# Kernel tuning notes

Measured on AMD Instinct MI355X. Metric: run time of the kernel, lower is better.

The kernel has to match this reference:

```python
import jax, jax.numpy as jnp
import numpy as np

# Model constants (match init_kwargs and fla GatedLinearAttention defaults used in source)
L = 4            # num_layers
D = 1024         # d_model
H = 4            # n_heads
DK = 128         # head key dim  = 0.5*D / H
DV = 256         # head value dim = 1.0*D / H
KD = H * DK      # total key dim = 512
VD = H * DV      # total value dim = 1024
V = 32000        # vocab
B, T = 1, 2048
LR = 16          # gate_low_rank_dim
GLN = 16.0       # gate_logit_normalizer
EPS = 1e-5
SCALE = DK ** -0.5


def setup_inputs() -> dict:
    key = jax.random.key(0)
    ks = jax.random.split(key, 12)
    s = 0.02
    return {
        "input_ids": jax.random.randint(ks[0], (B, T), 0, V),
        "emb": jax.random.normal(ks[1], (V, D), jnp.float32) * s,
        "Wq": jax.random.normal(ks[2], (L, D, KD), jnp.float32) * s,
        "Wk": jax.random.normal(ks[3], (L, D, KD), jnp.float32) * s,
        "Wv": jax.random.normal(ks[4], (L, D, VD), jnp.float32) * s,
        "Wg": jax.random.normal(ks[5], (L, D, VD), jnp.float32) * s,
        "Wgk1": jax.random.normal(ks[6], (L, D, LR), jnp.float32) * s,
        "Wgk2": jax.random.normal(ks[7], (L, LR, KD), jnp.float32) * s,
        "bgk": jnp.zeros((L, KD), jnp.float32),
        "gnw": jnp.ones((L, DV), jnp.float32),
        "Wo": jax.random.normal(ks[8], (L, VD, D), jnp.float32) * s,
        "ln_w": jnp.ones((D,), jnp.float32),
        "ln_b": jnp.zeros((D,), jnp.float32),
        "Wlm": jax.random.normal(ks[9], (D, V), jnp.float32) * s,
        "blm": jnp.zeros((V,), jnp.float32),
    }


def _gla_layer(x, wq, wk, wv, wg, wg1, wg2, bg, nw, wo):
    # x: [B, T, D]
    b, t, _ = x.shape
    q = (x @ wq).reshape(b, t, H, DK) * SCALE
    k = (x @ wk).reshape(b, t, H, DK)
    v = (x @ wv).reshape(b, t, H, DV)
    g = (x @ wg).reshape(b, t, H, DV)
    # low-rank forget gate, log-space, normalized
    gk = (jax.nn.log_sigmoid((x @ wg1) @ wg2 + bg) / GLN).reshape(b, t, H, DK)

    # time-major for scan: [T, B, H, *]
    qt, kt, vt, gkt = (jnp.moveaxis(a, 1, 0) for a in (q, k, v, gk))

    def step(S, inp):
        q_t, k_t, v_t, gk_t = inp  # [B,H,DK], [B,H,DK], [B,H,DV], [B,H,DK]
        S = S * jnp.exp(gk_t)[..., None] + k_t[..., None] * v_t[..., None, :]
        o_t = jnp.einsum('bhk,bhkv->bhv', q_t, S)
        return S, o_t

    S0 = jnp.zeros((b, H, DK, DV), x.dtype)
    _, o = jax.lax.scan(step, S0, (qt, kt, vt, gkt))
    o = jnp.moveaxis(o, 0, 1)  # [B, T, H, DV]
    # fused RMSNorm + swish output gate
    o = o * jax.lax.rsqrt(jnp.mean(o * o, axis=-1, keepdims=True) + EPS) * nw
    o = o * (g * jax.nn.sigmoid(g))
    return o.reshape(b, t, VD) @ wo


def reference(input_ids, emb, Wq, Wk, Wv, Wg, Wgk1, Wgk2, bgk, gnw, Wo, ln_w, ln_b, Wlm, blm):
    h = emb[input_ids]  # [B, T, D]
    for i in range(L):
        h = _gla_layer(h, Wq[i], Wk[i], Wv[i], Wg[i], Wgk1[i], Wgk2[i], bgk[i], gnw[i], Wo[i])
    mu = jnp.mean(h, axis=-1, keepdims=True)
    var = jnp.mean((h - mu) ** 2, axis=-1, keepdims=True)
    h = (h - mu) * jax.lax.rsqrt(var + EPS) * ln_w + ln_b
    return h @ Wlm + blm
```

## Files before the change

### kernel.cpp

```cpp
#include <hip/hip_runtime.h>
#include <hip/hip_bf16.h>
#include <math.h>

#define NL 4
#define TT 2048
#define DD 1024
#define KDIM 512
#define VDIM 1024
#define QSTR 3072
#define NH 4
#define DKH 128
#define DVH 256
#define CH 64
#define NCH 32
#define VOCAB 32000
#define SCALE_Q 0.08838834764831845f

typedef short bf16x8 __attribute__((ext_vector_type(8)));
typedef float f32x4 __attribute__((ext_vector_type(4)));

__device__ __forceinline__ void gload_lds16(const void* g, void* l) {
    __builtin_amdgcn_global_load_lds((const __attribute__((address_space(1))) void*)g,
                                     (__attribute__((address_space(3))) void*)l, 16, 0, 0);
}

__device__ __forceinline__ void store_bf16x4(__hip_bfloat16* p, float a, float b, float c, float d) {
    union { __hip_bfloat16 h[4]; ushort4 v; } r;
    r.h[0] = __float2bfloat16(a); r.h[1] = __float2bfloat16(b);
    r.h[2] = __float2bfloat16(c); r.h[3] = __float2bfloat16(d);
    *(ushort4*)p = r.v;
}

__global__ __launch_bounds__(256) void embed_kernel(const int* __restrict__ ids,
                                                    const float* __restrict__ emb,
                                                    float* __restrict__ h,
                                                    __hip_bfloat16* __restrict__ hb) {
    int idx = blockIdx.x * 256 + threadIdx.x;
    int t = idx >> 8, c4 = idx & 255;
    float4 v = *(const float4*)(emb + (size_t)ids[t] * DD + c4 * 4);
    *(float4*)(h + (size_t)t * DD + c4 * 4) = v;
    store_bf16x4(hb + (size_t)t * DD + c4 * 4, v.x, v.y, v.z, v.w);
}

__global__ __launch_bounds__(256) void tconv_kernel(const float* __restrict__ in,
                                                    __hip_bfloat16* __restrict__ out,
                                                    int K, int N) {
    __shared__ float tle[64][65];
    const int n0 = blockIdx.x * 64, k0 = blockIdx.y * 64;
    const int tid = threadIdx.x;
    const int ty = tid >> 4, tx = tid & 15;
#pragma unroll
    for (int u = 0; u < 4; u++) {
        int r = ty + u * 16;
        float4 v = *(const float4*)(in + (size_t)(k0 + r) * N + n0 + tx * 4);
        tle[r][tx * 4 + 0] = v.x; tle[r][tx * 4 + 1] = v.y;
        tle[r][tx * 4 + 2] = v.z; tle[r][tx * 4 + 3] = v.w;
    }
    __syncthreads();
#pragma unroll
    for (int u = 0; u < 4; u++) {
        int nn = u * 16 + ty;
        store_bf16x4(out + (size_t)(n0 + nn) * K + k0 + tx * 4,
                     tle[tx * 4 + 0][nn], tle[tx * 4 + 1][nn],
                     tle[tx * 4 + 2][nn], tle[tx * 4 + 3][nn]);
    }
}

__global__ __launch_bounds__(256) void tconv_layer_kernel(const float* __restrict__ wq,
                                                          const float* __restrict__ wk,
                                                          const float* __restrict__ wv,
                                                          const float* __restrict__ wg,
                                                          const float* __restrict__ wo,
                                                          __hip_bfloat16* __restrict__ Wt,
                                                          __hip_bfloat16* __restrict__ WoT) {
    __shared__ float tle[64][65];
    int b = blockIdx.x;
    const float* src; __hip_bfloat16* dst; int N, local;
    if (b < 128)      { src = wq; dst = Wt;                         N = 512;  local = b; }
    else if (b < 256) { src = wk; dst = Wt + (size_t)512 * 1024;    N = 512;  local = b - 128; }
    else if (b < 512) { src = wv; dst = Wt + (size_t)1024 * 1024;   N = 1024; local = b - 256; }
    else if (b < 768) { src = wg; dst = Wt + (size_t)2048 * 1024;   N = 1024; local = b - 512; }
    else              { src = wo; dst = WoT;                        N = 1024; local = b - 768; }
    int nbx = N >> 6;
    int n0 = (local % nbx) * 64, k0 = (local / nbx) * 64;
    const int tid = threadIdx.x;
    const int ty = tid >> 4, tx = tid & 15;
#pragma unroll
    for (int u = 0; u < 4; u++) {
        int r = ty + u * 16;
        float4 v = *(const float4*)(src + (size_t)(k0 + r) * N + n0 + tx * 4);
        tle[r][tx * 4 + 0] = v.x; tle[r][tx * 4 + 1] = v.y;
        tle[r][tx * 4 + 2] = v.z; tle[r][tx * 4 + 3] = v.w;
    }
    __syncthreads();
#pragma unroll
    for (int u = 0; u < 4; u++) {
        int nn = u * 16 + ty;
        store_bf16x4(dst + (size_t)(n0 + nn) * 1024 + k0 + tx * 4,
                     tle[tx * 4 + 0][nn], tle[tx * 4 + 1][nn],
                     tle[tx * 4 + 2][nn], tle[tx * 4 + 3][nn]);
    }
}

template<int NF>
__global__ __launch_bounds__(256) void gemm_bf16_db(const __hip_bfloat16* __restrict__ A,
                                                    const __hip_bfloat16* __restrict__ Bt,
                                                    const float* __restrict__ bias,
                                                    float* __restrict__ C,
                                                    __hip_bfloat16* __restrict__ Cb,
                                                    int M, int N, int K) {
    __shared__ short a_lds[2][128 * 32];
    __shared__ short b_lds[2][NF * 32 * 32];
    const int tid = threadIdx.x;
    const int wv = tid >> 6, lane = tid & 63;
    const int wr = wv >> 1, wc = wv & 1;
    const int nbx = gridDim.x;
    int wg = blockIdx.y * nbx + blockIdx.x;
    int cpx = (nbx * gridDim.y) >> 3;
    int swz = (wg & 7) * cpx + (wg >> 3);
    const int m0 = (swz % nbx) * 128, n0 = (swz / nbx) * (NF * 32);
    const int lr = lane & 15, lk = (lane >> 4) * 8;

    f32x4 acc[4][NF];
#pragma unroll
    for (int m = 0; m < 4; m++)
#pragma unroll
        for (int n = 0; n < NF; n++) acc[m][n] = (f32x4)(0.f);

    auto STAGE = [&](int buf, int k0) {
#pragma unroll
        for (int u = 0; u < 2; u++) {
            int s = wv * 128 + u * 64 + lane;
            int r = s >> 2, kc = (s & 3) * 8;
            gload_lds16(A + (size_t)(m0 + r) * K + k0 + kc,
                        &a_lds[buf][(wv * 128 + u * 64) * 8]);
        }
        if constexpr (NF == 4) {
#pragma unroll
            for (int u = 0; u < 2; u++) {
                int s = wv * 128 + u * 64 + lane;
                int r = s >> 2, kc = (s & 3) * 8;
                gload_lds16(Bt + (size_t)(n0 + r) * K + k0 + kc,
                            &b_lds[buf][(wv * 128 + u * 64) * 8]);
            }
        } else {
            int s = wv * 64 + lane;
            int r = s >> 2, kc = (s & 3) * 8;
            gload_lds16(Bt + (size_t)(n0 + r) * K + k0 + kc,
                        &b_lds[buf][(wv * 64) * 8]);
        }
    };
    auto COMPUTE = [&](int buf) {
        bf16x8 af[4], bfr[NF];
#pragma unroll
        for (int m = 0; m < 4; m++)
            af[m] = *(const bf16x8*)&a_lds[buf][(wr * 64 + m * 16 + lr) * 32 + lk];
#pragma unroll
        for (int n = 0; n < NF; n++)
            bfr[n] = *(const bf16x8*)&b_lds[buf][(wc * (NF * 16) + n * 16 + lr) * 32 + lk];
#pragma unroll
        for (int m = 0; m < 4; m++)
#pragma unroll
            for (int n = 0; n < NF; n++)
                acc[m][n] = __builtin_amdgcn_mfma_f32_16x16x32_bf16(af[m], bfr[n], acc[m][n], 0, 0, 0);
    };

    STAGE(0, 0);
    __syncthreads();
    int cur = 0;
    for (int k0 = 32; k0 < K; k0 += 32) {
        STAGE(cur ^ 1, k0);
        COMPUTE(cur);
        __syncthreads();
        cur ^= 1;
    }
    COMPUTE(cur);

    const int rbase = (lane >> 4) * 4;
#pragma unroll
    for (int n = 0; n < NF; n++) {
        int col = n0 + wc * (NF * 16) + n * 16 + lr;
        float bv = bias ? bias[col] : 0.f;
#pragma unroll
        for (int m = 0; m < 4; m++) {
            int row = m0 + wr * 64 + m * 16 + rbase;
#pragma unroll
            for (int r = 0; r < 4; r++) {
                float val = acc[m][n][r] + bv;
                C[(size_t)(row + r) * N + col] = val;
                if (Cb) Cb[(size_t)(row + r) * N + col] = __float2bfloat16(val);
            }
        }
    }
}

__device__ __forceinline__ void lm_stage(const __hip_bfloat16* src, int row0,
                                         char* dst, int kt32, int wv, int lane, int K) {
#pragma unroll
    for (int ii = 0; ii < 2; ii++) {
        int o = (wv * 2 + ii) * 1024;
        int ob = o + lane * 16;
        int lg = ob ^ (((ob >> 7) & 7) << 4);
        int row = lg >> 6;
        int ce = (lg & 63) >> 1;
        gload_lds16(src + (size_t)(row0 + row) * K + kt32 * 32 + ce, dst + o);
    }
}

__device__ __forceinline__ bf16x8 lm_frag(const char* sub, int row, int lk2) {
    int lg = ((row >> 1) << 7) + ((row & 1) << 6) + lk2;
    return *(const bf16x8*)(sub + (lg ^ (((row >> 1) & 7) << 4)));
}

template<int PT, bool LOADB, int VM>
__device__ __forceinline__ void lm_phase(const char* aT, const char* bT,
                                         const __hip_bfloat16* ssrc, int srow0,
                                         char* sdst, int skt32,
                                         bf16x8 (&bfr)[4][2], f32x4 (&acc)[8][4],
                                         int wr, int wc, int lr, int lk2,
                                         int wv, int lane, int K) {
    if constexpr (LOADB) {
#pragma unroll
        for (int n = 0; n < 4; n++)
#pragma unroll
            for (int ks = 0; ks < 2; ks++)
                bfr[n][ks] = lm_frag(bT + ks * 16384, wc * 64 + n * 16 + lr, lk2);
    }
    bf16x8 af[2][2];
#pragma unroll
    for (int mm = 0; mm < 2; mm++)
#pragma unroll
        for (int ks = 0; ks < 2; ks++)
            af[mm][ks] = lm_frag(aT + ks * 16384, wr * 128 + (2 * PT + mm) * 16 + lr, lk2);
    lm_stage(ssrc, srow0, sdst, skt32, wv, lane, K);
    asm volatile("s_barrier" ::: "memory");
    __builtin_amdgcn_s_setprio(1);
#pragma unroll
    for (int mm = 0; mm < 2; mm++)
#pragma unroll
        for (int n = 0; n < 4; n++) {
            acc[2 * PT + mm][n] = __builtin_amdgcn_mfma_f32_16x16x32_bf16(af[mm][0], bfr[n][0], acc[2 * PT + mm][n], 0, 0, 0);
            acc[2 * PT + mm][n] = __builtin_amdgcn_mfma_f32_16x16x32_bf16(af[mm][1], bfr[n][1], acc[2 * PT + mm][n], 0, 0, 0);
        }
    __builtin_amdgcn_s_setprio(0);
    if constexpr (VM == 4) asm volatile("s_waitcnt vmcnt(4)" ::: "memory");
    asm volatile("s_barrier" ::: "memory");
}

__global__ __launch_bounds__(512, 1) void gemm256_lm(const __hip_bfloat16* __restrict__ A,
                                                     const __hip_bfloat16* __restrict__ Bt,
                                                     const float* __restrict__ bias,
                                                     float* __restrict__ C,
                                                     int M, int N, int K) {
    extern __shared__ __align__(16) char smem[];
    char* sA0 = smem;
    char* sA1 = smem + 32768;
    char* sB0 = smem + 65536;
    char* sB1 = smem + 98304;
    const int tid = threadIdx.x;
    const int wv = tid >> 6, lane = tid & 63;
    const int wr = wv >> 2, wc = wv & 3;
    const int lr = lane & 15, lk2 = (lane >> 4) * 16;

    const int nbx = gridDim.x;
    int wg = blockIdx.y * nbx + blockIdx.x;
    int cpx = (nbx * gridDim.y) >> 3;
    int swz = (wg & 7) * cpx + (wg >> 3);
    const int m0 = (swz % nbx) * 256;
    const int n0 = (swz / nbx) * 256;

    f32x4 acc[8][4];
#pragma unroll
    for (int m = 0; m < 8; m++)
#pragma unroll
        for (int n = 0; n < 4; n++) acc[m][n] = (f32x4)(0.f);

    const int NTI = K / 64;
    const int NI  = NTI / 2;

    lm_stage(A,  m0, sA0 + 0,     0, wv, lane, K);
    lm_stage(A,  m0, sA0 + 16384, 1, wv, lane, K);
    lm_stage(Bt, n0, sB0 + 0,     0, wv, lane, K);
    lm_stage(Bt, n0, sB0 + 16384, 1, wv, lane, K);
    lm_stage(Bt, n0, sB1 + 0,     2, wv, lane, K);
    lm_stage(Bt, n0, sB1 + 16384, 3, wv, lane, K);
    asm volatile("s_waitcnt vmcnt(0)" ::: "memory");
    asm volatile("s_barrier" ::: "memory");

    for (int i = 0; i < NI; i++) {
        int tOdd = 2 * i + 1;
        int tE   = 2 * i + 2 < NTI ? 2 * i + 2 : NTI - 1;
        int tB3  = 2 * i + 3 < NTI ? 2 * i + 3 : NTI - 1;
        bf16x8 bfr[4][2];
        lm_phase<0, true , 0>(sA0, sB0, A,  m0, sA1 + 0,     2 * tOdd + 0, bfr, acc, wr, wc, lr, lk2, wv, lane, K);
        lm_phase<1, false, 0>(sA0, sB0, A,  m0, sA1 + 16384, 2 * tOdd + 1, bfr, acc, wr, wc, lr, lk2, wv, lane, K);
        lm_phase<2, false, 0>(sA0, sB0, Bt, n0, sB0 + 0,     2 * tE   + 0, bfr, acc, wr, wc, lr, lk2, wv, lane, K);
        lm_phase<3, false, 4>(sA0, sB0, Bt, n0, sB0 + 16384, 2 * tE   + 1, bfr, acc, wr, wc, lr, lk2, wv, lane, K);
        lm_phase<0, true , 0>(sA1, sB1, A,  m0, sA0 + 0,     2 * tE   + 0, bfr, acc, wr, wc, lr, lk2, wv, lane, K);
        lm_phase<1, false, 0>(sA1, sB1, A,  m0, sA0 + 16384, 2 * tE   + 1, bfr, acc, wr, wc, lr, lk2, wv, lane, K);
        lm_phase<2, false, 0>(sA1, sB1, Bt, n0, sB1 + 0,     2 * tB3  + 0, bfr, acc, wr, wc, lr, lk2, wv, lane, K);
        lm_phase<3, false, 4>(sA1, sB1, Bt, n0, sB1 + 16384, 2 * tB3  + 1, bfr, acc, wr, wc, lr, lk2, wv, lane, K);
    }

    const int r4 = (lane >> 4) * 4;
#pragma unroll
    for (int n = 0; n < 4; n++) {
        int col = n0 + wc * 64 + n * 16 + lr;
        float bv = bias ? bias[col] : 0.f;
#pragma unroll
        for (int m = 0; m < 8; m++) {
            int row = m0 + wr * 128 + m * 16 + r4;
#pragma unroll
            for (int r = 0; r < 4; r++)
                C[(size_t)(row + r) * N + col] = acc[m][n][r] + bv;
        }
    }
}

__global__ __launch_bounds__(256) void lowrank1_kernel(const float* __restrict__ h,
                                                       const float* __restrict__ W1,
                                                       float* __restrict__ xg) {
    int t = blockIdx.x;
    int tid = threadIdx.x;
    int j = tid & 15, ks = tid >> 4;
    const float* hr = h + (size_t)t * DD + ks * 64;
    const float* w = W1 + (size_t)(ks * 64) * 16 + j;
    float acc = 0.f;
#pragma unroll 8
    for (int kk = 0; kk < 64; kk++) acc = fmaf(hr[kk], w[kk * 16], acc);
    __shared__ float red[16][17];
    red[ks][j] = acc;
    __syncthreads();
    if (tid < 16) {
        float s = 0.f;
#pragma unroll
        for (int r = 0; r < 16; r++) s += red[r][tid];
        xg[t * 16 + tid] = s;
    }
}

__global__ __launch_bounds__(256) void lowrank2_kernel(const float* __restrict__ xg,
                                                       const float* __restrict__ W2,
                                                       const float* __restrict__ bg,
                                                       float* __restrict__ gk) {
    int idx = blockIdx.x * 256 + threadIdx.x;
    int t = idx >> 9, n = idx & 511;
    const float* xr = xg + t * 16;
    float s = bg[n];
#pragma unroll
    for (int r = 0; r < 16; r++) s = fmaf(xr[r], W2[r * KDIM + n], s);
    float ls = fminf(s, 0.f) - log1pf(expf(-fabsf(s)));
    gk[idx] = ls * (1.f / 16.f);
}

__global__ __launch_bounds__(256) void gatescan_kernel(const float* __restrict__ qkvg,
                                                       const float* __restrict__ gk,
                                                       float* __restrict__ Gl,
                                                       __hip_bfloat16* __restrict__ qhB,
                                                       __hip_bfloat16* __restrict__ khB,
                                                       __hip_bfloat16* __restrict__ ktT) {
    int idx = blockIdx.x * 256 + threadIdx.x;
    int c = idx >> 9, col = idx & 511;
    float G = 0.f;
    float kh[64];
#pragma unroll
    for (int t = 0; t < 64; t++) {
        G += gk[(size_t)(c * 64 + t) * KDIM + col];
        const float* qp = qkvg + (size_t)(c * 64 + t) * QSTR + col;
        float qv = qp[0], kv = qp[512];
        qhB[(size_t)(c * 64 + t) * KDIM + col] = __float2bfloat16(qv * expf(G) * SCALE_Q);
        float khv = kv * expf(-G);
        khB[(size_t)(c * 64 + t) * KDIM + col] = __float2bfloat16(khv);
        kh[t] = khv;
    }
    Gl[idx] = G;
    float eGl = expf(G);
    int hh = col >> 7, dk = col & 127;
    __hip_bfloat16* kp = ktT + ((size_t)(c * NH + hh) * DKH + dk) * CH;
#pragma unroll
    for (int t = 0; t < 64; t++) kp[t] = __float2bfloat16(kh[t] * eGl);
}

__global__ __launch_bounds__(256) void vtrans_kernel(const float* __restrict__ qkvg,
                                                     __hip_bfloat16* __restrict__ vT) {
    __shared__ float tle[64][65];
    int bid = blockIdx.x;
    int dvq = bid & 3, hh = (bid >> 2) & 3, c = bid >> 4;
    int tid = threadIdx.x, ty = tid >> 4, tx = tid & 15;
#pragma unroll
    for (int u = 0; u < 4; u++) {
        int r = u * 16 + ty;
        float4 v = *(const float4*)(qkvg + (size_t)(c * 64 + r) * QSTR + 1024 + hh * DVH + dvq * 64 + tx * 4);
        tle[r][tx * 4 + 0] = v.x; tle[r][tx * 4 + 1] = v.y;
        tle[r][tx * 4 + 2] = v.z; tle[r][tx * 4 + 3] = v.w;
    }
    __syncthreads();
    __hip_bfloat16* dst = vT + ((size_t)(c * NH + hh) * DVH + dvq * 64) * CH;
#pragma unroll
    for (int u = 0; u < 4; u++) {
        int dv = u * 16 + ty;
        store_bf16x4(dst + (size_t)dv * CH + tx * 4,
                     tle[tx * 4 + 0][dv], tle[tx * 4 + 1][dv],
                     tle[tx * 4 + 2][dv], tle[tx * 4 + 3][dv]);
    }
}

__global__ __launch_bounds__(256) void chunkU_mfma(const __hip_bfloat16* __restrict__ vT,
                                                   const __hip_bfloat16* __restrict__ ktT,
                                                   __hip_bfloat16* __restrict__ U) {
    const int ch = blockIdx.x;
    const __hip_bfloat16* Ap = vT + (size_t)ch * DVH * CH;
    const __hip_bfloat16* Bp = ktT + (size_t)ch * DKH * CH;
    __hip_bfloat16* Cp = U + (size_t)ch * DVH * DKH;
    const int tid = threadIdx.x, wv = tid >> 6, lane = tid & 63;
    const int wr = wv >> 1, wc = wv & 1;
    const int lr = lane & 15, lk = (lane >> 4) * 8;
    f32x4 acc[8][4];
#pragma unroll
    for (int m = 0; m < 8; m++)
#pragma unroll
        for (int n = 0; n < 4; n++) acc[m][n] = (f32x4)(0.f);
#pragma unroll
    for (int ks = 0; ks < 2; ks++) {
        bf16x8 a[8], b[4];
#pragma unroll
        for (int m = 0; m < 8; m++)
            a[m] = *(const bf16x8*)(Ap + (size_t)(wr * 128 + m * 16 + lr) * CH + ks * 32 + lk);
#pragma unroll
        for (int n = 0; n < 4; n++)
            b[n] = *(const bf16x8*)(Bp + (size_t)(wc * 64 + n * 16 + lr) * CH + ks * 32 + lk);
#pragma unroll
        for (int m = 0; m < 8; m++)
#pragma unroll
            for (int n = 0; n < 4; n++)
                acc[m][n] = __builtin_amdgcn_mfma_f32_16x16x32_bf16(a[m], b[n], acc[m][n], 0, 0, 0);
    }
    const int r4 = (lane >> 4) * 4;
#pragma unroll
    for (int m = 0; m < 8; m++)
#pragma unroll
        for (int n = 0; n < 4; n++)
#pragma unroll
            for (int r = 0; r < 4; r++)
                Cp[(size_t)(wr * 128 + m * 16 + r4 + r) * DKH + wc * 64 + n * 16 + lr] =
                    __float2bfloat16(acc[m][n][r]);
}

__global__ __launch_bounds__(256) void scan_states_kernel(__hip_bfloat16* __restrict__ U,
                                                          const float* __restrict__ Gl) {
    int idx = blockIdx.x * 256 + threadIdx.x;
    int hh = idx >> 15, dv = (idx >> 7) & 255, dk = idx & 127;
    int col = hh * DKH + dk;
    float s = 0.f;
    for (int c = 0; c < NCH; c++) {
        __hip_bfloat16* p = U + ((size_t)(c * NH + hh) * DVH + dv) * DKH + dk;
        float u = __bfloat162float(*p);
        *p = __float2bfloat16(s);
        s = s * expf(Gl[c * KDIM + col]) + u;
    }
}

__global__ __launch_bounds__(256) void attn_rms_mfma(const __hip_bfloat16* __restrict__ qhB,
                                                     const __hip_bfloat16* __restrict__ khB,
                                                     const __hip_bfloat16* __restrict__ vT,
                                                     const __hip_bfloat16* __restrict__ Ub,
                                                     const float* __restrict__ qkvg,
                                                     const float* __restrict__ nw,
                                                     __hip_bfloat16* __restrict__ obb) {
    __shared__ __hip_bfloat16 P[32 * 72];
    __shared__ float sums[32][2];
    const int bid = blockIdx.x;
    const int rh = bid & 1, hh = (bid >> 1) & 3, c = bid >> 3;
    const int t0 = c * CH;
    const int tid = threadIdx.x, wv = tid >> 6, lane = tid & 63;
    const int half = wv >> 1, rg = wv & 1;
    const int lr = lane & 15, lk = (lane >> 4) * 8;
    const int r4 = (lane >> 4) * 4;
    const int rr = rh * 32 + rg * 16;

    bf16x8 qf[4];
#pragma unroll
    for (int ks = 0; ks < 4; ks++)
        qf[ks] = *(const bf16x8*)(qhB + (size_t)(t0 + rr + lr) * KDIM + hh * DKH + ks * 32 + lk);

    if (half == 0) {
        f32x4 s[4];
#pragma unroll
        for (int n = 0; n < 4; n++) s[n] = (f32x4)(0.f);
#pragma unroll
        for (int n = 0; n < 4; n++)
#pragma unroll
            for (int ks = 0; ks < 4; ks++) {
                bf16x8 kf = *(const bf16x8*)(khB + (size_t)(t0 + n * 16 + lr) * KDIM + hh * DKH + ks * 32 + lk);
                s[n] = __builtin_amdgcn_mfma_f32_16x16x32_bf16(qf[ks], kf, s[n], 0, 0, 0);
            }
#pragma unroll
        for (int n = 0; n < 4; n++)
#pragma unroll
            for (int r = 0; r < 4; r++) {
                int i = rr + r4 + r, j = n * 16 + lr;
                float val = (j <= i) ? s[n][r] : 0.f;
                P[(rg * 16 + r4 + r) * 72 + j] = __float2bfloat16(val);
            }
    }
    __syncthreads();

    const __hip_bfloat16* vTp = vT + ((size_t)(c * NH + hh) * DVH + half * 128) * CH;
    const __hip_bfloat16* Ubp = Ub + ((size_t)(c * NH + hh) * DVH + half * 128) * DKH;
    bf16x8 pf[2];
#pragma unroll
    for (int ks = 0; ks < 2; ks++)
        pf[ks] = *(const bf16x8*)&P[(rg * 16 + lr) * 72 + ks * 32 + lk];

    f32x4 o[8];
#pragma unroll
    for (int n = 0; n < 8; n++) o[n] = (f32x4)(0.f);
#pragma unroll
    for (int n = 0; n < 8; n++) {
#pragma unroll
        for (int ks = 0; ks < 2; ks++) {
            bf16x8 vf = *(const bf16x8*)(vTp + (size_t)(n * 16 + lr) * CH + ks * 32 + lk);
            o[n] = __builtin_amdgcn_mfma_f32_16x16x32_bf16(pf[ks], vf, o[n], 0, 0, 0);
        }
#pragma unroll
        for (int ks = 0; ks < 4; ks++) {
            bf16x8 uf = *(const bf16x8*)(Ubp + (size_t)(n * 16 + lr) * DKH + ks * 32 + lk);
            o[n] = __builtin_amdgcn_mfma_f32_16x16x32_bf16(qf[ks], uf, o[n], 0, 0, 0);
        }
    }

    float part[4];
#pragma unroll
    for (int r = 0; r < 4; r++) {
        float p = 0.f;
#pragma unroll
        for (int n = 0; n < 8; n++) p = fmaf(o[n][r], o[n][r], p);
        part[r] = p;
    }
#pragma unroll
    for (int off = 1; off < 16; off <<= 1)
#pragma unroll
        for (int r = 0; r < 4; r++) part[r] += __shfl_xor(part[r], off);
    if (lr == 0)
#pragma unroll
        for (int r = 0; r < 4; r++) sums[rg * 16 + r4 + r][half] = part[r];
    __syncthreads();

#pragma unroll
    for (int r = 0; r < 4; r++) {
        int lrow = rg * 16 + r4 + r;
        int t = t0 + rh * 32 + lrow;
        float tot = sums[lrow][0] + sums[lrow][1];
        float rinv = rsqrtf(tot * (1.f / 256.f) + 1e-5f);
#pragma unroll
        for (int n = 0; n < 8; n++) {
            int col = half * 128 + n * 16 + lr;
            float gv = qkvg[(size_t)t * QSTR + 2048 + hh * DVH + col];
            float val = o[n][r] * rinv * nw[col] * (gv / (1.f + expf(-gv)));
            obb[(size_t)t * VDIM + hh * DVH + col] = __float2bfloat16(val);
        }
    }
}

__global__ __launch_bounds__(256) void ln_kernel(const float* __restrict__ h,
                                                 const float* __restrict__ w,
                                                 const float* __restrict__ b,
                                                 __hip_bfloat16* __restrict__ out16) {
    int t = blockIdx.x;
    int tid = threadIdx.x;
    float4 x = *(const float4*)(h + (size_t)t * DD + tid * 4);
    float s = x.x + x.y + x.z + x.w;
    float ss = x.x * x.x + x.y * x.y + x.z * x.z + x.w * x.w;
#pragma unroll
    for (int off = 32; off > 0; off >>= 1) {
        s += __shfl_xor(s, off);
        ss += __shfl_xor(ss, off);
    }
    __shared__ float rs[4], rss[4];
    int wv = tid >> 6;
    if ((tid & 63) == 0) { rs[wv] = s; rss[wv] = ss; }
    __syncthreads();
    s = rs[0] + rs[1] + rs[2] + rs[3];
    ss = rss[0] + rss[1] + rss[2] + rss[3];
    float mu = s * (1.f / 1024.f);
    float var = ss * (1.f / 1024.f) - mu * mu;
    float r = rsqrtf(var + 1e-5f);
    float4 wv4 = *(const float4*)(w + tid * 4);
    float4 bv4 = *(const float4*)(b + tid * 4);
    store_bf16x4(out16 + (size_t)t * DD + tid * 4,
                 (x.x - mu) * r * wv4.x + bv4.x,
                 (x.y - mu) * r * wv4.y + bv4.y,
                 (x.z - mu) * r * wv4.z + bv4.z,
                 (x.w - mu) * r * wv4.w + bv4.w);
}

extern "C" void kernel_launch(void* const* d_in, const int* in_sizes, int n_in,
                              void* d_out, int out_size, void* d_ws, size_t ws_size,
                              hipStream_t stream) {
    const int*   ids  = (const int*)d_in[0];
    const float* emb  = (const float*)d_in[1];
    const float* Wq   = (const float*)d_in[2];
    const float* Wk   = (const float*)d_in[3];
    const float* Wv   = (const float*)d_in[4];
    const float* Wg   = (const float*)d_in[5];
    const float* Wgk1 = (const float*)d_in[6];
    const float* Wgk2 = (const float*)d_in[7];
    const float* bgk  = (const float*)d_in[8];
    const float* gnw  = (const float*)d_in[9];
    const float* Wo   = (const float*)d_in[10];
    const float* lnw  = (const float*)d_in[11];
    const float* lnb  = (const float*)d_in[12];
    const float* Wlm  = (const float*)d_in[13];
    const float* blm  = (const float*)d_in[14];
    float* out = (float*)d_out;

    float* ws = (float*)d_ws;
    float* h    = ws; ws += (size_t)TT * DD;
    float* qkvg = ws; ws += (size_t)TT * QSTR;
    float* gk   = ws; ws += (size_t)TT * KDIM;
    float* xg   = ws; ws += (size_t)TT * 16;
    float* Gl   = ws; ws += (size_t)NCH * KDIM;
    __hip_bfloat16* hb    = (__hip_bfloat16*)ws; ws += (size_t)TT * DD / 2;
    __hip_bfloat16* obb   = (__hip_bfloat16*)ws; ws += (size_t)TT * DD / 2;
    __hip_bfloat16* lnb16 = (__hip_bfloat16*)ws; ws += (size_t)TT * DD / 2;
    __hip_bfloat16* qhB   = (__hip_bfloat16*)ws; ws += (size_t)TT * KDIM / 2;
    __hip_bfloat16* khB   = (__hip_bfloat16*)ws; ws += (size_t)TT * KDIM / 2;
    __hip_bfloat16* ktT   = (__hip_bfloat16*)ws; ws += (size_t)NCH * NH * DKH * CH / 2;
    __hip_bfloat16* vT    = (__hip_bfloat16*)ws; ws += (size_t)NCH * NH * DVH * CH / 2;
    __hip_bfloat16* Ub    = (__hip_bfloat16*)ws; ws += (size_t)NCH * NH * DVH * DKH / 2;
    __hip_bfloat16* Wt    = (__hip_bfloat16*)ws; ws += (size_t)QSTR * DD / 2;
    __hip_bfloat16* WoT   = (__hip_bfloat16*)ws; ws += (size_t)VDIM * DD / 2;
    __hip_bfloat16* WlmT  = (__hip_bfloat16*)ws; ws += (size_t)VOCAB * DD / 2;

    hipFuncSetAttribute((const void*)gemm256_lm,
                        hipFuncAttributeMaxDynamicSharedMemorySize, 131072);

    embed_kernel<<<TT, 256, 0, stream>>>(ids, emb, h, hb);
    tconv_kernel<<<dim3(VOCAB / 64, DD / 64), 256, 0, stream>>>(Wlm, WlmT, DD, VOCAB);

    for (int l = 0; l < NL; l++) {
        const float* w1 = Wgk1 + (size_t)l * DD * 16;
        const float* w2 = Wgk2 + (size_t)l * 16 * KDIM;
        const float* bg = bgk + (size_t)l * KDIM;
        const float* nw = gnw + (size_t)l * DVH;

        tconv_layer_kernel<<<1024, 256, 0, stream>>>(Wq + (size_t)l * DD * KDIM,
                                                     Wk + (size_t)l * DD * KDIM,
                                                     Wv + (size_t)l * DD * VDIM,
                                                     Wg + (size_t)l * DD * VDIM,
                                                     Wo + (size_t)l * VDIM * DD, Wt, WoT);
        gemm_bf16_db<4><<<dim3(TT / 128, QSTR / 128), 256, 0, stream>>>(hb, Wt, nullptr, qkvg, nullptr, TT, QSTR, DD);
        lowrank1_kernel<<<TT, 256, 0, stream>>>(h, w1, xg);
        lowrank2_kernel<<<TT * KDIM / 256, 256, 0, stream>>>(xg, w2, bg, gk);
        gatescan_kernel<<<NCH * KDIM / 256, 256, 0, stream>>>(qkvg, gk, Gl, qhB, khB, ktT);
        vtrans_kernel<<<NCH * NH * 4, 256, 0, stream>>>(qkvg, vT);
        chunkU_mfma<<<NCH * NH, 256, 0, stream>>>(vT, ktT, Ub);
        scan_states_kernel<<<NH * DVH * DKH / 256, 256, 0, stream>>>(Ub, Gl);
        attn_rms_mfma<<<NCH * NH * 2, 256, 0, stream>>>(qhB, khB, vT, Ub, qkvg, nw, obb);
        gemm_bf16_db<2><<<dim3(TT / 128, DD / 64), 256, 0, stream>>>(obb, WoT, nullptr, h, hb, TT, DD, VDIM);
    }

    ln_kernel<<<TT, 256, 0, stream>>>(h, lnw, lnb, lnb16);
    gemm256_lm<<<dim3(TT / 256, VOCAB / 256), 512, 131072, stream>>>(lnb16, WlmT, blm, out, TT, VOCAB, DD);
}
```

Measured before the change: 706.1 us.

## Fuse low-rank gate projection into chunked gate scan and relax LM-head vmcnt wait

Merges the second low-rank gate kernel into the gate cumulative-sum kernel. Each block now computes log-sigmoid gates for a 64-token chunk and 64 columns from shared-memory copies of W2 and xg, then forms the prefix sums with a four-way segmented scan. This removes the gk intermediate buffer round-trip and one launch per layer. It also splits the serial 64-step scan across four thread groups and vectorizes the ktT writes. Separately, the LM-head GEMM's vmcnt wait threshold is changed from 4 to 2, which makes it wait for more outstanding loads before the barrier.

```diff
diff --git a/kernel.cpp b/kernel.cpp
--- a/kernel.cpp
+++ b/kernel.cpp
@@ -243,7 +243,7 @@
             acc[2 * PT + mm][n] = __builtin_amdgcn_mfma_f32_16x16x32_bf16(af[mm][1], bfr[n][1], acc[2 * PT + mm][n], 0, 0, 0);
         }
     __builtin_amdgcn_s_setprio(0);
-    if constexpr (VM == 4) asm volatile("s_waitcnt vmcnt(4)" ::: "memory");
+    if constexpr (VM == 2) asm volatile("s_waitcnt vmcnt(2)" ::: "memory");
     asm volatile("s_barrier" ::: "memory");
 }
 
@@ -295,11 +295,11 @@
         lm_phase<0, true , 0>(sA0, sB0, A,  m0, sA1 + 0,     2 * tOdd + 0, bfr, acc, wr, wc, lr, lk2, wv, lane, K);
         lm_phase<1, false, 0>(sA0, sB0, A,  m0, sA1 + 16384, 2 * tOdd + 1, bfr, acc, wr, wc, lr, lk2, wv, lane, K);
         lm_phase<2, false, 0>(sA0, sB0, Bt, n0, sB0 + 0,     2 * tE   + 0, bfr, acc, wr, wc, lr, lk2, wv, lane, K);
-        lm_phase<3, false, 4>(sA0, sB0, Bt, n0, sB0 + 16384, 2 * tE   + 1, bfr, acc, wr, wc, lr, lk2, wv, lane, K);
+        lm_phase<3, false, 2>(sA0, sB0, Bt, n0, sB0 + 16384, 2 * tE   + 1, bfr, acc, wr, wc, lr, lk2, wv, lane, K);
         lm_phase<0, true , 0>(sA1, sB1, A,  m0, sA0 + 0,     2 * tE   + 0, bfr, acc, wr, wc, lr, lk2, wv, lane, K);
         lm_phase<1, false, 0>(sA1, sB1, A,  m0, sA0 + 16384, 2 * tE   + 1, bfr, acc, wr, wc, lr, lk2, wv, lane, K);
         lm_phase<2, false, 0>(sA1, sB1, Bt, n0, sB1 + 0,     2 * tB3  + 0, bfr, acc, wr, wc, lr, lk2, wv, lane, K);
-        lm_phase<3, false, 4>(sA1, sB1, Bt, n0, sB1 + 16384, 2 * tB3  + 1, bfr, acc, wr, wc, lr, lk2, wv, lane, K);
+        lm_phase<3, false, 2>(sA1, sB1, Bt, n0, sB1 + 16384, 2 * tB3  + 1, bfr, acc, wr, wc, lr, lk2, wv, lane, K);
     }
 
     const int r4 = (lane >> 4) * 4;
@@ -339,46 +339,72 @@
     }
 }
 
-__global__ __launch_bounds__(256) void lowrank2_kernel(const float* __restrict__ xg,
-                                                       const float* __restrict__ W2,
-                                                       const float* __restrict__ bg,
-                                                       float* __restrict__ gk) {
-    int idx = blockIdx.x * 256 + threadIdx.x;
-    int t = idx >> 9, n = idx & 511;
-    const float* xr = xg + t * 16;
-    float s = bg[n];
-#pragma unroll
-    for (int r = 0; r < 16; r++) s = fmaf(xr[r], W2[r * KDIM + n], s);
-    float ls = fminf(s, 0.f) - log1pf(expf(-fabsf(s)));
-    gk[idx] = ls * (1.f / 16.f);
-}
-
-__global__ __launch_bounds__(256) void gatescan_kernel(const float* __restrict__ qkvg,
-                                                       const float* __restrict__ gk,
-                                                       float* __restrict__ Gl,
-                                                       __hip_bfloat16* __restrict__ qhB,
-                                                       __hip_bfloat16* __restrict__ khB,
-                                                       __hip_bfloat16* __restrict__ ktT) {
-    int idx = blockIdx.x * 256 + threadIdx.x;
-    int c = idx >> 9, col = idx & 511;
-    float G = 0.f;
-    float kh[64];
-#pragma unroll
-    for (int t = 0; t < 64; t++) {
-        G += gk[(size_t)(c * 64 + t) * KDIM + col];
-        const float* qp = qkvg + (size_t)(c * 64 + t) * QSTR + col;
+__global__ __launch_bounds__(256) void gatefuse2_kernel(const float* __restrict__ qkvg,
+                                                        const float* __restrict__ xg,
+                                                        const float* __restrict__ W2,
+                                                        const float* __restrict__ bg,
+                                                        float* __restrict__ Gl,
+                                                        __hip_bfloat16* __restrict__ qhB,
+                                                        __hip_bfloat16* __restrict__ khB,
+                                                        __hip_bfloat16* __restrict__ ktT) {
+    __shared__ float w2s[16][64];
+    __shared__ float xgs[64][16];
+    __shared__ float part[4][64];
+    const int tid = threadIdx.x;
+    const int j = tid & 63, sg = tid >> 6;
+    const int cg = blockIdx.x & 7, c = blockIdx.x >> 3;
+    const int col = cg * 64 + j;
+#pragma unroll
+    for (int r = 0; r < 4; r++)
+        w2s[sg * 4 + r][j] = W2[(size_t)(sg * 4 + r) * KDIM + col];
+#pragma unroll
+    for (int u = 0; u < 4; u++) {
+        int id = u * 256 + tid;
+        int t = id >> 4, r = id & 15;
+        xgs[t][r] = xg[(size_t)(c * 64 + t) * 16 + r];
+    }
+    __syncthreads();
+    const float bgv = bg[col];
+    float ls[16];
+    float partial = 0.f;
+#pragma unroll
+    for (int i = 0; i < 16; i++) {
+        int t = sg * 16 + i;
+        float s = bgv;
+#pragma unroll
+        for (int r = 0; r < 16; r++) s = fmaf(xgs[t][r], w2s[r][j], s);
+        float v = (fminf(s, 0.f) - log1pf(expf(-fabsf(s)))) * (1.f / 16.f);
+        ls[i] = v;
+        partial += v;
+    }
+    part[sg][j] = partial;
+    __syncthreads();
+    float base = 0.f, total = 0.f;
+#pragma unroll
+    for (int r = 0; r < 4; r++) {
+        float p = part[r][j];
+        if (r < sg) base += p;
+        total += p;
+    }
+    if (sg == 0) Gl[c * KDIM + col] = total;
+    const float eGl = expf(total);
+    const int hh = col >> 7, dk = col & 127;
+    __hip_bfloat16 ktbuf[16];
+    float G = base;
+#pragma unroll
+    for (int i = 0; i < 16; i++) {
+        int t = c * 64 + sg * 16 + i;
+        G += ls[i];
+        const float* qp = qkvg + (size_t)t * QSTR + col;
         float qv = qp[0], kv = qp[512];
-        qhB[(size_t)(c * 64 + t) * KDIM + col] = __float2bfloat16(qv * expf(G) * SCALE_Q);
+        qhB[(size_t)t * KDIM + col] = __float2bfloat16(qv * expf(G) * SCALE_Q);
         float khv = kv * expf(-G);
-        khB[(size_t)(c * 64 + t) * KDIM + col] = __float2bfloat16(khv);
-        kh[t] = khv;
-    }
-    Gl[idx] = G;
-    float eGl = expf(G);
-    int hh = col >> 7, dk = col & 127;
-    __hip_bfloat16* kp = ktT + ((size_t)(c * NH + hh) * DKH + dk) * CH;
-#pragma unroll
-    for (int t = 0; t < 64; t++) kp[t] = __float2bfloat16(kh[t] * eGl);
+        khB[(size_t)t * KDIM + col] = __float2bfloat16(khv);
+        ktbuf[i] = __float2bfloat16(khv * eGl);
+    }
+    __hip_bfloat16* kp = ktT + ((size_t)(c * NH + hh) * DKH + dk) * CH + sg * 16;
+    *(uint4*)(kp + 0) = *(uint4*)&ktbuf[0];
+    *(uint4*)(kp + 8) = *(uint4*)&ktbuf[8];
 }
 
 __global__ __launch_bounds__(256) void vtrans_kernel(const float* __restrict__ qkvg,
@@ -617,7 +643,6 @@
     float* ws = (float*)d_ws;
     float* h    = ws; ws += (size_t)TT * DD;
     float* qkvg = ws; ws += (size_t)TT * QSTR;
-    float* gk   = ws; ws += (size_t)TT * KDIM;
     float* xg   = ws; ws += (size_t)TT * 16;
     float* Gl   = ws; ws += (size_t)NCH * KDIM;
     __hip_bfloat16* hb    = (__hip_bfloat16*)ws; ws += (size_t)TT * DD / 2;
@@ -651,8 +676,7 @@
                                                      Wo + (size_t)l * VDIM * DD, Wt, WoT);
         gemm_bf16_db<4><<<dim3(TT / 128, QSTR / 128), 256, 0, stream>>>(hb, Wt, nullptr, qkvg, nullptr, TT, QSTR, DD);
         lowrank1_kernel<<<TT, 256, 0, stream>>>(h, w1, xg);
-        lowrank2_kernel<<<TT * KDIM / 256, 256, 0, stream>>>(xg, w2, bg, gk);
-        gatescan_kernel<<<NCH * KDIM / 256, 256, 0, stream>>>(qkvg, gk, Gl, qhB, khB, ktT);
+        gatefuse2_kernel<<<NCH * (KDIM / 64), 256, 0, stream>>>(qkvg, xg, w2, bg, Gl, qhB, khB, ktT);
         vtrans_kernel<<<NCH * NH * 4, 256, 0, stream>>>(qkvg, vT);
         chunkU_mfma<<<NCH * NH, 256, 0, stream>>>(vT, ktT, Ub);
         scan_states_kernel<<<NH * DVH * DKH / 256, 256, 0, stream>>>(Ub, Gl);
```

Result: faster. 660.6 us (-6.4%).
